# Performance work log

Measured on AMD Instinct MI355X. Metric: run time of the kernel, lower is better.

## Reference

```python
import jax, jax.numpy as jnp
import numpy as np

N_HEADS = 16  # must match init_kwargs
BIAS_SCALE = 0.1


def _src_grid(out_size, in_size):
    # torch F.interpolate bilinear, align_corners=False semantics
    scale = in_size / out_size
    src = jnp.clip((jnp.arange(out_size, dtype=jnp.float32) + 0.5) * scale - 0.5, 0.0)
    i0 = jnp.minimum(jnp.floor(src).astype(jnp.int32), in_size - 1)
    i1 = jnp.minimum(i0 + 1, in_size - 1)
    w = src - i0.astype(jnp.float32)
    return i0, i1, w


def _bilinear_resize(img, out_h, out_w):
    Hin, Win = img.shape[-2], img.shape[-1]
    r0, r1, wy = _src_grid(out_h, Hin)
    c0, c1, wx = _src_grid(out_w, Win)
    rows = img[:, r0, :] * (1.0 - wy)[None, :, None] + img[:, r1, :] * wy[None, :, None]
    return rows[:, :, c0] * (1.0 - wx)[None, None, :] + rows[:, :, c1] * wx[None, None, :]


def setup_inputs() -> dict:
    key = jax.random.key(0)
    ks = jax.random.split(key, 10)
    B, L, D, M, K = 4, 1024, 1024, 64, 32
    s = 0.02
    return {
        "x": jax.random.normal(ks[0], (B, L, D), dtype=jnp.float32),
        "harmonics": jax.random.normal(ks[1], (B, M, K), dtype=jnp.float32),
        "wq": jax.random.normal(ks[2], (D, D), dtype=jnp.float32) * s,
        "bq": jax.random.normal(ks[3], (D,), dtype=jnp.float32) * s,
        "wk": jax.random.normal(ks[4], (D, D), dtype=jnp.float32) * s,
        "bk": jax.random.normal(ks[5], (D,), dtype=jnp.float32) * s,
        "wv": jax.random.normal(ks[6], (D, D), dtype=jnp.float32) * s,
        "bv": jax.random.normal(ks[7], (D,), dtype=jnp.float32) * s,
        "wo": jax.random.normal(ks[8], (D, D), dtype=jnp.float32) * s,
        "bo": jax.random.normal(ks[9], (D,), dtype=jnp.float32) * s,
    }


def reference(x, harmonics, wq, bq, wk, bk, wv, bv, wo, bo):
    B, L, D = x.shape
    hd = D // N_HEADS
    scaling = hd ** -0.5

    def split_heads(t):  # [B, L, D] -> [B, H, L, hd]
        return t.reshape(B, L, N_HEADS, hd).transpose(0, 2, 1, 3)

    q = split_heads(x @ wq.T + bq)
    k = split_heads(x @ wk.T + bk)
    v = split_heads(x @ wv.T + bv)

    scores = jnp.einsum("bhqd,bhkd->bhqk", q, k) * scaling  # [B, H, L, L]

    gram = jnp.einsum("bmk,bnk->bmn", harmonics, harmonics)  # [B, M, M]
    bias = _bilinear_resize(gram, L, L)  # [B, L, L]
    scores = scores + BIAS_SCALE * bias[:, None, :, :]

    attn = jax.nn.softmax(scores, axis=-1)
    out = jnp.einsum("bhqk,bhkd->bhqd", attn, v)  # [B, H, L, hd]
    out = out.transpose(0, 2, 1, 3).reshape(B, L, D)
    return out @ wo.T + bo
```

## Files before the change

kernel.cpp:

```cpp
#include <hip/hip_runtime.h>


using short8  = __attribute__((ext_vector_type(8))) short;
using short4v = __attribute__((ext_vector_type(4))) short;
using float4v = __attribute__((ext_vector_type(4))) float;

#define MFMA16(a, b, c) __builtin_amdgcn_mfma_f32_16x16x32_bf16((a), (b), (c), 0, 0, 0)

#define LOG2E 1.44269504088896f

static __device__ __forceinline__ short f2bf(float f) {
    union { float f; unsigned u; } v; v.f = f;
    unsigned r = v.u + 0x7fffu + ((v.u >> 16) & 1u);
    return (short)(r >> 16);
}

static __device__ __forceinline__ unsigned pack2bf(float lo, float hi) {
    union { float f; unsigned u; } a, b;
    a.f = lo; b.f = hi;
    return __builtin_amdgcn_perm(b.u + 0x8000u, a.u + 0x8000u, 0x07060302u);
}

static __device__ __forceinline__ void dma16(const short* g, short* l) {
    __builtin_amdgcn_global_load_lds((const __attribute__((address_space(1))) void*)g,
                                     (__attribute__((address_space(3))) void*)l, 16, 0, 0);
}

__global__ __launch_bounds__(256) void convert_bf16(const float* __restrict__ in,
                                                    short* __restrict__ out, int n4) {
    int idx = blockIdx.x * 256 + threadIdx.x;
    for (int i = idx; i < n4; i += gridDim.x * 256) {
        float4v v = *(const float4v*)(in + (size_t)i * 4);
        short4v o;
        o.x = f2bf(v.x); o.y = f2bf(v.y); o.z = f2bf(v.z); o.w = f2bf(v.w);
        *(short4v*)(out + (size_t)i * 4) = o;
    }
}

__global__ __launch_bounds__(256) void convert_w4(const float* __restrict__ w0,
                                                  const float* __restrict__ w1,
                                                  const float* __restrict__ w2,
                                                  const float* __restrict__ w3,
                                                  short* __restrict__ out) {
    int z = blockIdx.y;
    const float* w = (z == 0) ? w0 : (z == 1) ? w1 : (z == 2) ? w2 : w3;
    short* o = out + (size_t)z * 1048576;
    int idx = blockIdx.x * 256 + threadIdx.x;
    for (int i = idx; i < 262144; i += gridDim.x * 256) {
        float4v v = *(const float4v*)(w + (size_t)i * 4);
        short4v s;
        s.x = f2bf(v.x); s.y = f2bf(v.y); s.z = f2bf(v.z); s.w = f2bf(v.w);
        *(short4v*)(o + (size_t)i * 4) = s;
    }
}

__global__ __launch_bounds__(256) void gram_kernel(const float* __restrict__ harm,
                                                   float* __restrict__ gram) {
    int b = blockIdx.x;
    __shared__ float hs[64][32];
    int tid = threadIdx.x;
    for (int i = tid; i < 2048; i += 256) hs[i >> 5][i & 31] = harm[(size_t)b * 2048 + i];
    __syncthreads();
    for (int i = tid; i < 4096; i += 256) {
        int m = i >> 6, n = i & 63;
        float s = 0.f;
        #pragma unroll
        for (int k = 0; k < 32; k++) s += hs[m][k] * hs[n][k];
        gram[(size_t)b * 4096 + i] = s;
    }
}

__global__ __launch_bounds__(256) void fill_aug(const float* __restrict__ gram,
                                                short* __restrict__ Qp,
                                                short* __restrict__ Kp) {
    int b  = blockIdx.y;
    int lc = blockIdx.x;
    int tid = threadIdx.x;
    int ll = tid >> 3;
    int d8 = (tid & 7) * 8;
    int l  = lc * 32 + ll;

    float src = (l + 0.5f) * 0.0625f - 0.5f;
    if (src < 0.f) src = 0.f;
    int r0 = (int)floorf(src); if (r0 > 63) r0 = 63;
    int r1 = r0 + 1;           if (r1 > 63) r1 = 63;
    float wy = src - (float)r0;

    const float* g0 = gram + ((size_t)b * 64 + r0) * 64 + d8;
    const float* g1 = gram + ((size_t)b * 64 + r1) * 64 + d8;
    short8 qa, ka;
    #pragma unroll
    for (int j = 0; j < 8; j++)
        qa[j] = f2bf(0.1f * LOG2E * (g0[j] * (1.f - wy) + g1[j] * wy));
    #pragma unroll
    for (int j = 0; j < 8; j++) {
        float vv = 0.f;
        if (d8 + j == r0) vv += 1.f - wy;
        if (d8 + j == r1) vv += wy;
        ka[j] = f2bf(vv);
    }
    for (int h = 0; h < 16; h++) {
        size_t base = (((size_t)(b * 16 + h) * 1024 + l) << 7) + 64 + d8;
        *(short8*)(Qp + base) = qa;
        *(short8*)(Kp + base) = ka;
    }
}

template <int MODE>
__global__ __launch_bounds__(256, 2) void gemm_kernel(
    const short* __restrict__ A,
    const short* __restrict__ Wb,
    const float* __restrict__ B0, const float* __restrict__ B1, const float* __restrict__ B2,
    short* __restrict__ Qp, short* __restrict__ Kp, short* __restrict__ Vp,
    float* __restrict__ outF) {
    const int z = blockIdx.z;
    const short* W  = Wb + (size_t)z * 1048576;
    const float* Bs = (z == 0) ? B0 : ((z == 1) ? B1 : B2);

    __shared__ short As[128][40];
    __shared__ short Bsh[128][40];

    const int tid  = threadIdx.x;
    const int lane = tid & 63;
    const int wv   = tid >> 6;
    const int wm   = (wv >> 1) * 64;
    const int wn   = (wv & 1) * 64;
    const int l16  = lane & 15;
    const int quad = lane >> 4;
    const int bm   = blockIdx.x * 128;
    const int bn   = blockIdx.y * 128;

    float4v zero4 = {0.f, 0.f, 0.f, 0.f};
    float4v acc[4][4];
    #pragma unroll
    for (int i = 0; i < 4; i++)
        #pragma unroll
        for (int j = 0; j < 4; j++) acc[i][j] = zero4;

    for (int kt = 0; kt < 1024; kt += 32) {
        #pragma unroll
        for (int c = tid; c < 512; c += 256) {
            int r = c >> 2, c8 = (c & 3) * 8;
            *(short8*)&As[r][c8]  = *(const short8*)(A + (size_t)(bm + r) * 1024 + kt + c8);
            *(short8*)&Bsh[r][c8] = *(const short8*)(W + (size_t)(bn + r) * 1024 + kt + c8);
        }
        __syncthreads();
        short8 af[4], bfr[4];
        #pragma unroll
        for (int mt = 0; mt < 4; mt++) af[mt]  = *(const short8*)&As[wm + mt * 16 + l16][quad * 8];
        #pragma unroll
        for (int nt = 0; nt < 4; nt++) bfr[nt] = *(const short8*)&Bsh[wn + nt * 16 + l16][quad * 8];
        #pragma unroll
        for (int mt = 0; mt < 4; mt++)
            #pragma unroll
            for (int nt = 0; nt < 4; nt++)
                acc[mt][nt] = MFMA16(af[mt], bfr[nt], acc[mt][nt]);
        __syncthreads();
    }

    #pragma unroll
    for (int mt = 0; mt < 4; mt++)
        #pragma unroll
        for (int nt = 0; nt < 4; nt++) {
            int col = bn + wn + nt * 16 + l16;
            float bias = Bs[col];
            #pragma unroll
            for (int r = 0; r < 4; r++) {
                int row = bm + wm + mt * 16 + quad * 4 + r;
                float val = acc[mt][nt][r] + bias;
                if (MODE == 1) {
                    outF[(size_t)row * 1024 + col] = val;
                } else {
                    int b = row >> 10, l = row & 1023;
                    int h = col >> 6,  d = col & 63;
                    size_t bhl = (size_t)(b * 16 + h) * 1024 + l;
                    if (z == 0)      Qp[(bhl << 7) + d] = f2bf(val * (0.125f * LOG2E));
                    else if (z == 1) Kp[(bhl << 7) + d] = f2bf(val);
                    else {
                        int slot = (l & ~31) | (((l >> 2) & 3) << 3) |
                                   (((l >> 4) & 1) << 2) | (l & 3);
                        Vp[(((size_t)(b * 16 + h) * 64 + d) << 10) + slot] = f2bf(val);
                    }
                }
            }
        }
}

__global__ __attribute__((amdgpu_flat_work_group_size(256, 256),
                          amdgpu_waves_per_eu(2, 2)))
void flash_kernel(const short* __restrict__ Qp,
                  const short* __restrict__ Kp,
                  const short* __restrict__ Vp,
                  short* __restrict__ AO) {
    const int h  = blockIdx.x;
    const int qb = blockIdx.y;
    const int b  = blockIdx.z;
    const int tid  = threadIdx.x;
    const int lane = tid & 63;
    const int w    = tid >> 6;
    const int l16  = lane & 15;
    const int quad = lane >> 4;
    const size_t bh = (size_t)(b * 16 + h);

    __shared__ short Ks[16384];
    __shared__ short Vs[8192];

    short8 qf[2][4];
    #pragma unroll
    for (int n = 0; n < 2; n++) {
        const short* Qb = Qp + ((bh * 1024 + qb * 128 + w * 32 + n * 16 + l16) << 7) + quad * 8;
        #pragma unroll
        for (int c = 0; c < 4; c++) qf[n][c] = *(const short8*)(Qb + c * 32);
    }

    const short* kSrc[4];
    #pragma unroll
    for (int jj = 0; jj < 4; jj++) {
        int key = (w * 4 + jj) * 4 + quad;
        kSrc[jj] = Kp + (bh << 17) + key * 128 + ((l16 ^ (key & 15)) * 8);
    }
    const short* vSrc[2];
    #pragma unroll
    for (int jj = 0; jj < 2; jj++) {
        int d = (w * 2 + jj) * 8 + (lane >> 3);
        vSrc[jj] = Vp + (bh << 16) + d * 1024 + (((lane & 7) ^ (d & 7)) * 8);
    }

    int krd[4], vrd[2];
    #pragma unroll
    for (int c = 0; c < 4; c++) krd[c] = l16 * 128 + (((c * 4 + quad) ^ l16) * 8);
    #pragma unroll
    for (int g = 0; g < 2; g++) vrd[g] = l16 * 64 + (((g * 4 + quad) ^ (l16 & 7)) * 8);

    #pragma unroll
    for (int jj = 0; jj < 4; jj++) dma16(kSrc[jj], &Ks[w * 2048 + jj * 512]);
    #pragma unroll
    for (int jj = 0; jj < 2; jj++) dma16(vSrc[jj], &Vs[w * 1024 + jj * 512]);
    #pragma unroll
    for (int jj = 0; jj < 4; jj++) kSrc[jj] += 8192;
    #pragma unroll
    for (int jj = 0; jj < 2; jj++) vSrc[jj] += 64;
    int dstK = 8192, dstV = 4096;

    float4v zero4 = {0.f, 0.f, 0.f, 0.f};
    float4v o_acc[4][2];
    #pragma unroll
    for (int mt = 0; mt < 4; mt++)
        #pragma unroll
        for (int n = 0; n < 2; n++) o_acc[mt][n] = zero4;
    float l_part[2] = {0.f, 0.f};

    __syncthreads();

    for (int kt = 0; kt < 16; kt++) {
        if (kt < 15) {
            #pragma unroll
            for (int jj = 0; jj < 4; jj++) dma16(kSrc[jj], &Ks[dstK + w * 2048 + jj * 512]);
            #pragma unroll
            for (int jj = 0; jj < 2; jj++) dma16(vSrc[jj], &Vs[dstV + w * 1024 + jj * 512]);
            #pragma unroll
            for (int jj = 0; jj < 4; jj++) kSrc[jj] += 8192;
            #pragma unroll
            for (int jj = 0; jj < 2; jj++) vSrc[jj] += 64;
            dstK ^= 8192; dstV ^= 4096;
        }

        short8 vf[4][2];
        #pragma unroll
        for (int mt = 0; mt < 4; mt++)
            #pragma unroll
            for (int g = 0; g < 2; g++)
                vf[mt][g] = *(const short8*)&Vs[vrd[g] + mt * 1024];

        float4v s[4][2];
        #pragma unroll
        for (int mt = 0; mt < 4; mt++) {
            short8 kf[4];
            #pragma unroll
            for (int c = 0; c < 4; c++) kf[c] = *(const short8*)&Ks[krd[c] + mt * 2048];
            #pragma unroll
            for (int n = 0; n < 2; n++) {
                s[mt][n] = zero4;
                #pragma unroll
                for (int c = 0; c < 4; c++)
                    s[mt][n] = MFMA16(kf[c], qf[n][c], s[mt][n]);
            }
        }

        #pragma unroll
        for (int mt = 0; mt < 4; mt++)
            #pragma unroll
            for (int n = 0; n < 2; n++)
                #pragma unroll
                for (int r = 0; r < 4; r++) {
                    float p = __builtin_exp2f(s[mt][n][r]);
                    s[mt][n][r] = p;
                    l_part[n] += p;
                }

        #pragma unroll
        for (int g = 0; g < 2; g++) {
            short8 pf[2];
            #pragma unroll
            for (int n = 0; n < 2; n++) {
                union { unsigned u[4]; short8 v; } t;
                t.u[0] = pack2bf(s[2 * g][n][0], s[2 * g][n][1]);
                t.u[1] = pack2bf(s[2 * g][n][2], s[2 * g][n][3]);
                t.u[2] = pack2bf(s[2 * g + 1][n][0], s[2 * g + 1][n][1]);
                t.u[3] = pack2bf(s[2 * g + 1][n][2], s[2 * g + 1][n][3]);
                pf[n] = t.v;
            }
            #pragma unroll
            for (int mt = 0; mt < 4; mt++)
                #pragma unroll
                for (int n = 0; n < 2; n++)
                    o_acc[mt][n] = MFMA16(vf[mt][g], pf[n], o_acc[mt][n]);
        }

        if (kt < 15) __syncthreads();
        #pragma unroll
        for (int c = 0; c < 4; c++) krd[c] ^= 8192;
        #pragma unroll
        for (int g = 0; g < 2; g++) vrd[g] ^= 4096;
    }

    #pragma unroll
    for (int n = 0; n < 2; n++) {
        float l = l_part[n];
        l += __shfl_xor(l, 16, 64);
        l += __shfl_xor(l, 32, 64);
        float inv = 1.0f / l;
        int row = b * 1024 + qb * 128 + w * 32 + n * 16 + l16;
        #pragma unroll
        for (int mt = 0; mt < 4; mt++) {
            short4v ov;
            #pragma unroll
            for (int r = 0; r < 4; r++) ov[r] = f2bf(o_acc[mt][n][r] * inv);
            *(short4v*)(AO + (size_t)row * 1024 + h * 64 + mt * 16 + quad * 4) = ov;
        }
    }
}

extern "C" void kernel_launch(void* const* d_in, const int* in_sizes, int n_in,
                              void* d_out, int out_size, void* d_ws, size_t ws_size,
                              hipStream_t stream) {
    const float* x    = (const float*)d_in[0];
    const float* harm = (const float*)d_in[1];
    const float* wq   = (const float*)d_in[2];
    const float* bq   = (const float*)d_in[3];
    const float* wk   = (const float*)d_in[4];
    const float* bk   = (const float*)d_in[5];
    const float* wv   = (const float*)d_in[6];
    const float* bv   = (const float*)d_in[7];
    const float* wo   = (const float*)d_in[8];
    const float* bo   = (const float*)d_in[9];
    float* outF = (float*)d_out;

    short* xb   = (short*)d_ws;
    short* Qp   = xb + (size_t)4 * 1048576;
    short* Kp   = Qp + (size_t)8 * 1048576;
    short* Vp   = Kp + (size_t)8 * 1048576;
    short* Wqkv = Vp + (size_t)4 * 1048576;
    short* Wob  = Wqkv + (size_t)3 * 1048576;
    float* gram = (float*)(Wob + 1048576);
    short* AO   = xb;

    convert_bf16<<<dim3(1024), dim3(256), 0, stream>>>(x, xb, 1048576);
    convert_w4<<<dim3(256, 4), dim3(256), 0, stream>>>(wq, wk, wv, wo, Wqkv);
    gram_kernel<<<dim3(4), dim3(256), 0, stream>>>(harm, gram);
    gemm_kernel<0><<<dim3(32, 8, 3), dim3(256), 0, stream>>>(
        xb, Wqkv, bq, bk, bv, Qp, Kp, Vp, nullptr);
    fill_aug<<<dim3(32, 4), dim3(256), 0, stream>>>(gram, Qp, Kp);
    flash_kernel<<<dim3(16, 8, 4), dim3(256), 0, stream>>>(Qp, Kp, Vp, AO);
    gemm_kernel<1><<<dim3(32, 8, 1), dim3(256), 0, stream>>>(
        AO, Wob, bo, nullptr, nullptr, nullptr, nullptr, nullptr, outF);
}
```

Measured before the change: 217.2 us.

## Merge conversion kernels, fold gram into fill_aug, use async LDS DMA in GEMM

```diff
diff --git a/kernel.cpp b/kernel.cpp
--- a/kernel.cpp
+++ b/kernel.cpp
@@ -26,51 +26,31 @@
                                      (__attribute__((address_space(3))) void*)l, 16, 0, 0);
 }
 
-__global__ __launch_bounds__(256) void convert_bf16(const float* __restrict__ in,
-                                                    short* __restrict__ out, int n4) {
+__global__ __launch_bounds__(256) void convert_all(
+    const float* __restrict__ x,  const float* __restrict__ wq,
+    const float* __restrict__ wk, const float* __restrict__ wv,
+    const float* __restrict__ wo, short* __restrict__ xb, short* __restrict__ wb) {
     int idx = blockIdx.x * 256 + threadIdx.x;
-    for (int i = idx; i < n4; i += gridDim.x * 256) {
-        float4v v = *(const float4v*)(in + (size_t)i * 4);
+    for (int i = idx; i < 2097152; i += gridDim.x * 256) {
+        const float* src; short* dst;
+        if (i < 1048576) {
+            src = x + (size_t)i * 4;
+            dst = xb + (size_t)i * 4;
+        } else {
+            int j = i - 1048576;
+            int sel = j >> 18;
+            const float* w = (sel == 0) ? wq : (sel == 1) ? wk : (sel == 2) ? wv : wo;
+            src = w + (size_t)(j & 262143) * 4;
+            dst = wb + (size_t)j * 4;
+        }
+        float4v v = *(const float4v*)src;
         short4v o;
         o.x = f2bf(v.x); o.y = f2bf(v.y); o.z = f2bf(v.z); o.w = f2bf(v.w);
-        *(short4v*)(out + (size_t)i * 4) = o;
-    }
-}
-
-__global__ __launch_bounds__(256) void convert_w4(const float* __restrict__ w0,
-                                                  const float* __restrict__ w1,
-                                                  const float* __restrict__ w2,
-                                                  const float* __restrict__ w3,
-                                                  short* __restrict__ out) {
-    int z = blockIdx.y;
-    const float* w = (z == 0) ? w0 : (z == 1) ? w1 : (z == 2) ? w2 : w3;
-    short* o = out + (size_t)z * 1048576;
-    int idx = blockIdx.x * 256 + threadIdx.x;
-    for (int i = idx; i < 262144; i += gridDim.x * 256) {
-        float4v v = *(const float4v*)(w + (size_t)i * 4);
-        short4v s;
-        s.x = f2bf(v.x); s.y = f2bf(v.y); s.z = f2bf(v.z); s.w = f2bf(v.w);
-        *(short4v*)(o + (size_t)i * 4) = s;
-    }
-}
-
-__global__ __launch_bounds__(256) void gram_kernel(const float* __restrict__ harm,
-                                                   float* __restrict__ gram) {
-    int b = blockIdx.x;
-    __shared__ float hs[64][32];
-    int tid = threadIdx.x;
-    for (int i = tid; i < 2048; i += 256) hs[i >> 5][i & 31] = harm[(size_t)b * 2048 + i];
-    __syncthreads();
-    for (int i = tid; i < 4096; i += 256) {
-        int m = i >> 6, n = i & 63;
-        float s = 0.f;
-        #pragma unroll
-        for (int k = 0; k < 32; k++) s += hs[m][k] * hs[n][k];
-        gram[(size_t)b * 4096 + i] = s;
-    }
-}
-
-__global__ __launch_bounds__(256) void fill_aug(const float* __restrict__ gram,
+        *(short4v*)dst = o;
+    }
+}
+
+__global__ __launch_bounds__(256) void fill_aug(const float* __restrict__ harm,
                                                 short* __restrict__ Qp,
                                                 short* __restrict__ Kp) {
     int b  = blockIdx.y;
@@ -80,18 +60,28 @@
     int d8 = (tid & 7) * 8;
     int l  = lc * 32 + ll;
 
+    __shared__ float hs[64][33];
+    for (int i = tid; i < 2048; i += 256) hs[i >> 5][i & 31] = harm[(size_t)b * 2048 + i];
+    __syncthreads();
+
     float src = (l + 0.5f) * 0.0625f - 0.5f;
     if (src < 0.f) src = 0.f;
     int r0 = (int)floorf(src); if (r0 > 63) r0 = 63;
     int r1 = r0 + 1;           if (r1 > 63) r1 = 63;
     float wy = src - (float)r0;
 
-    const float* g0 = gram + ((size_t)b * 64 + r0) * 64 + d8;
-    const float* g1 = gram + ((size_t)b * 64 + r1) * 64 + d8;
+    float hr[32];
+    #pragma unroll
+    for (int k = 0; k < 32; k++) hr[k] = (1.f - wy) * hs[r0][k] + wy * hs[r1][k];
+
     short8 qa, ka;
     #pragma unroll
-    for (int j = 0; j < 8; j++)
-        qa[j] = f2bf(0.1f * LOG2E * (g0[j] * (1.f - wy) + g1[j] * wy));
+    for (int j = 0; j < 8; j++) {
+        float g = 0.f;
+        #pragma unroll
+        for (int k = 0; k < 32; k++) g += hr[k] * hs[d8 + j][k];
+        qa[j] = f2bf(0.1f * LOG2E * g);
+    }
     #pragma unroll
     for (int j = 0; j < 8; j++) {
         float vv = 0.f;
@@ -117,8 +107,7 @@
     const short* W  = Wb + (size_t)z * 1048576;
     const float* Bs = (z == 0) ? B0 : ((z == 1) ? B1 : B2);
 
-    __shared__ short As[128][40];
-    __shared__ short Bsh[128][40];
+    __shared__ short Sm[8192];
 
     const int tid  = threadIdx.x;
     const int lane = tid & 63;
@@ -130,6 +119,23 @@
     const int bm   = blockIdx.x * 128;
     const int bn   = blockIdx.y * 128;
 
+    const short* aSrc[2];
+    const short* wSrc[2];
+    #pragma unroll
+    for (int j = 0; j < 2; j++) {
+        int c = j * 256 + tid;
+        int r = c >> 2, gs = (c & 3) ^ (r & 3);
+        aSrc[j] = A + (size_t)(bm + r) * 1024 + gs * 8;
+        wSrc[j] = W + (size_t)(bn + r) * 1024 + gs * 8;
+    }
+    const int fr = ((quad ^ (l16 & 3)) * 8);
+    int ai[4], bi[4];
+    #pragma unroll
+    for (int t = 0; t < 4; t++) {
+        ai[t] = (wm + t * 16 + l16) * 32 + fr;
+        bi[t] = 4096 + (wn + t * 16 + l16) * 32 + fr;
+    }
+
     float4v zero4 = {0.f, 0.f, 0.f, 0.f};
     float4v acc[4][4];
     #pragma unroll
@@ -137,19 +143,20 @@
         #pragma unroll
         for (int j = 0; j < 4; j++) acc[i][j] = zero4;
 
-    for (int kt = 0; kt < 1024; kt += 32) {
-        #pragma unroll
-        for (int c = tid; c < 512; c += 256) {
-            int r = c >> 2, c8 = (c & 3) * 8;
-            *(short8*)&As[r][c8]  = *(const short8*)(A + (size_t)(bm + r) * 1024 + kt + c8);
-            *(short8*)&Bsh[r][c8] = *(const short8*)(W + (size_t)(bn + r) * 1024 + kt + c8);
-        }
+    for (int kt = 0; kt < 32; kt++) {
+        dma16(aSrc[0], &Sm[wv * 512]);
+        dma16(aSrc[1], &Sm[2048 + wv * 512]);
+        dma16(wSrc[0], &Sm[4096 + wv * 512]);
+        dma16(wSrc[1], &Sm[6144 + wv * 512]);
+        #pragma unroll
+        for (int j = 0; j < 2; j++) { aSrc[j] += 32; wSrc[j] += 32; }
         __syncthreads();
+
         short8 af[4], bfr[4];
         #pragma unroll
-        for (int mt = 0; mt < 4; mt++) af[mt]  = *(const short8*)&As[wm + mt * 16 + l16][quad * 8];
-        #pragma unroll
-        for (int nt = 0; nt < 4; nt++) bfr[nt] = *(const short8*)&Bsh[wn + nt * 16 + l16][quad * 8];
+        for (int mt = 0; mt < 4; mt++) af[mt]  = *(const short8*)&Sm[ai[mt]];
+        #pragma unroll
+        for (int nt = 0; nt < 4; nt++) bfr[nt] = *(const short8*)&Sm[bi[nt]];
         #pragma unroll
         for (int mt = 0; mt < 4; mt++)
             #pragma unroll
@@ -362,15 +369,12 @@
     short* Vp   = Kp + (size_t)8 * 1048576;
     short* Wqkv = Vp + (size_t)4 * 1048576;
     short* Wob  = Wqkv + (size_t)3 * 1048576;
-    float* gram = (float*)(Wob + 1048576);
     short* AO   = xb;
 
-    convert_bf16<<<dim3(1024), dim3(256), 0, stream>>>(x, xb, 1048576);
-    convert_w4<<<dim3(256, 4), dim3(256), 0, stream>>>(wq, wk, wv, wo, Wqkv);
-    gram_kernel<<<dim3(4), dim3(256), 0, stream>>>(harm, gram);
+    convert_all<<<dim3(2048), dim3(256), 0, stream>>>(x, wq, wk, wv, wo, xb, Wqkv);
     gemm_kernel<0><<<dim3(32, 8, 3), dim3(256), 0, stream>>>(
         xb, Wqkv, bq, bk, bv, Qp, Kp, Vp, nullptr);
-    fill_aug<<<dim3(32, 4), dim3(256), 0, stream>>>(gram, Qp, Kp);
+    fill_aug<<<dim3(32, 4), dim3(256), 0, stream>>>(harm, Qp, Kp);
     flash_kernel<<<dim3(16, 8, 4), dim3(256), 0, stream>>>(Qp, Kp, Vp, AO);
     gemm_kernel<1><<<dim3(32, 8, 1), dim3(256), 0, stream>>>(
         AO, Wob, bo, nullptr, nullptr, nullptr, nullptr, nullptr, outF);
```

Result: faster. 198.3 us (-8.7%).
